# Kernel tuning notes

Measured on AMD Instinct MI355X. Metric: run time of the kernel, lower is better.

Reference implementation:

```python
import jax, jax.numpy as jnp
import numpy as np

H = 16      # heads
D = 64      # head_dim
C = 64      # k_centroid
HID = H * D
TAU1 = 1.0
TAU2 = 1.0


def setup_inputs() -> dict:
    key = jax.random.key(0)
    ks = jax.random.split(key, 12)
    B, S = 4, 1024
    inv = 1.0 / np.sqrt(D)
    return {
        "query": jax.random.normal(ks[0], (B, S, HID), dtype=jnp.float32),
        "key": jax.random.normal(ks[1], (B, S, HID), dtype=jnp.float32),
        "value": jax.random.normal(ks[2], (B, S, HID), dtype=jnp.float32),
        "Wq": jax.random.uniform(ks[3], (D, D), jnp.float32, -inv, inv),
        "bq": jax.random.uniform(ks[4], (D,), jnp.float32, -inv, inv),
        "Wk": jax.random.uniform(ks[5], (D, D), jnp.float32, -inv, inv),
        "bk": jax.random.uniform(ks[6], (D,), jnp.float32, -inv, inv),
        "Wv": jax.random.uniform(ks[7], (D, D), jnp.float32, -inv, inv),
        "bv": jax.random.uniform(ks[8], (D,), jnp.float32, -inv, inv),
        "centroid": jax.random.uniform(ks[9], (D, C), jnp.float32, -0.5, 0.5),
        "Wfc": jax.random.uniform(ks[10], (HID, HID), jnp.float32, -1.0 / np.sqrt(HID), 1.0 / np.sqrt(HID)),
        "bfc": jax.random.uniform(ks[11], (HID,), jnp.float32, -1.0 / np.sqrt(HID), 1.0 / np.sqrt(HID)),
    }


def _forward(query, key, value, Wq, bq, Wk, bk, Wv, bv, centroid, Wfc, bfc):
    B, S, _ = query.shape
    q = query.reshape(B, S, H, D)
    k = key.reshape(B, S, H, D)
    v = value.reshape(B, S, H, D)
    # per-head linear projections (applied on last dim, nn.Linear equivalent)
    Q = jnp.einsum('nshd,de->nshe', q, Wq) + bq
    K = jnp.einsum('nshd,de->nshe', k, Wk) + bk
    V = jnp.einsum('nshd,de->nshe', v, Wv) + bv
    # VQ-style key quantization: project keys onto centroids, gumbel-softmax over codebook
    K_ = jnp.einsum('nshd,dc->nshc', K, centroid)            # [B,S,H,C]
    g1 = jax.random.gumbel(jax.random.key(42), K_.shape, dtype=K_.dtype)
    prob = jax.nn.softmax((K_ + g1) / TAU1, axis=-1)
    sto_K = jnp.einsum('nshc,dc->nshd', prob, centroid)      # prob @ centroid.T
    # gumbel-softmax attention over QK^T
    scores = jnp.einsum('nqhd,nkhd->nhqk', Q, sto_K)         # [B,H,S,S]
    g2 = jax.random.gumbel(jax.random.key(43), scores.shape, dtype=scores.dtype)
    attn = jax.nn.softmax((scores + g2) / TAU2, axis=3)
    out = jnp.einsum('nhql,nlhd->nqhd', attn, V).reshape(B, S, HID)
    return jnp.einsum('nsd,de->nse', out, Wfc) + bfc


def reference(query, key, value, Wq, bq, Wk, bk, Wv, bv, centroid, Wfc, bfc):
    return _forward(query, key, value, Wq, bq, Wk, bk, Wv, bv, centroid, Wfc, bfc)
```

## Files before the change

kernel.cpp:

```cpp
#include <hip/hip_runtime.h>
#include <hip/hip_bf16.h>
#include <cstdint>

typedef unsigned short u16;
typedef __attribute__((ext_vector_type(8))) short short8;
typedef __attribute__((ext_vector_type(4))) float f32x4;

#define LT 72
#define LOG2E 1.4426950408889634f

__device__ __forceinline__ u16 f2bf(float x) {
  __hip_bfloat16 h = __float2bfloat16(x);
  union { __hip_bfloat16 h; u16 u; } cv; cv.h = h; return cv.u;
}
__device__ __forceinline__ u16 f2bf_fast(float x) {
  uint32_t b = __float_as_uint(x);
  return (u16)((b + 0x7fffu + ((b >> 16) & 1u)) >> 16);
}
__device__ __forceinline__ float bf2f(u16 u) {
  union { u16 u; __hip_bfloat16 h; } cv; cv.u = u; return __bfloat162float(cv.h);
}
__device__ __forceinline__ float ld(const void* base, size_t i, int isb) {
  return isb ? bf2f(((const u16*)base)[i]) : ((const float*)base)[i];
}
__device__ __forceinline__ void st_out(void* base, size_t i, float v, int isb) {
  if (isb) ((u16*)base)[i] = f2bf_fast(v);
  else     ((float*)base)[i] = v;
}
__device__ __forceinline__ int probe_is_bf16(const void* q) {
  const u16* u = (const u16*)q;
  int sane = 0;
  for (int i = 0; i < 64; i++) {
    u16 x = u[2 * i];
    int e = (x >> 7) & 0xff;
    sane += (int)(((e >= 117) && (e <= 133)) || ((x & 0x7fff) == 0));
  }
  return sane >= 32;
}

__device__ __forceinline__ uint32_t rotl32(uint32_t x, int n) {
  return __builtin_amdgcn_alignbit(x, x, (uint32_t)(32 - n));
}
__device__ __forceinline__ void threefry4x(uint32_t k1, uint32_t x1base,
                                           uint32_t out[4]) {
  const uint32_t ks2 = k1 ^ 0x1BD11BDAu;
  uint32_t x0[4], x1[4];
  #pragma unroll
  for (int j = 0; j < 4; j++) { x0[j] = 0u; x1[j] = x1base + ((uint32_t)j << 4); }
#define R4(rot) \
  _Pragma("unroll") \
  for (int j = 0; j < 4; j++) { \
    x0[j] += x1[j]; x1[j] = rotl32(x1[j], rot); x1[j] ^= x0[j]; \
  }
  R4(13) R4(15) R4(26) R4(6)
  #pragma unroll
  for (int j = 0; j < 4; j++) { x0[j] += k1; x1[j] += ks2 + 1u; }
  R4(17) R4(29) R4(16) R4(24)
  #pragma unroll
  for (int j = 0; j < 4; j++) { x0[j] += ks2; x1[j] += 2u; }
  R4(13) R4(15) R4(26) R4(6)
  #pragma unroll
  for (int j = 0; j < 4; j++) { x1[j] += k1 + 3u; }
  R4(17) R4(29) R4(16) R4(24)
  #pragma unroll
  for (int j = 0; j < 4; j++) { x0[j] += k1; x1[j] += ks2 + 4u; }
  R4(13) R4(15) R4(26) R4(6)
  #pragma unroll
  for (int j = 0; j < 4; j++) { out[j] = (x0[j] + ks2) ^ (x1[j] + 5u); }
#undef R4
}
__device__ __forceinline__ float rcp_l2n(uint32_t bits) {
  float u = __uint_as_float(0x3f800000u | (bits >> 9)) - 1.0f;
  float l2n = -__log2f(u);
  float t = 1.0f - u;
  float fix = fmaf(0.5f * t, t, t) * LOG2E;
  l2n = (bits >= 0xFF000000u) ? fix : l2n;
  return __builtin_amdgcn_rcpf(l2n);
}
__device__ __forceinline__ float qsum(float v) {
  v += __shfl_xor(v, 1, 64);
  v += __shfl_xor(v, 2, 64);
  v += __shfl_xor(v, 4, 64);
  v += __shfl_xor(v, 8, 64);
  return v;
}
__device__ __forceinline__ void stage_tile(u16* dst, const u16* src,
                                           int src_stride, int tid) {
  #pragma unroll
  for (int i = 0; i < 2; i++) {
    int u = tid + (i << 8);
    int r = u >> 3, c8 = (u & 7) * 8;
    *(short8*)&dst[r * LT + c8] =
        *(const short8*)&src[(size_t)r * src_stride + c8];
  }
}
__device__ __forceinline__ void pf_tile(short8 regs[2], const u16* src,
                                        int src_stride, int tid) {
  #pragma unroll
  for (int i = 0; i < 2; i++) {
    int u = tid + (i << 8);
    int r = u >> 3, c8 = (u & 7) * 8;
    regs[i] = *(const short8*)&src[(size_t)r * src_stride + c8];
  }
}
__device__ __forceinline__ void flush_tile(u16* dst, const short8 regs[2],
                                           int tid) {
  #pragma unroll
  for (int i = 0; i < 2; i++) {
    int u = tid + (i << 8);
    int r = u >> 3, c8 = (u & 7) * 8;
    *(short8*)&dst[r * LT + c8] = regs[i];
  }
}
__device__ __forceinline__ void stage_x(u16* dst, const void* src, size_t base,
                                        int isb, int tid) {
  if (isb) {
    const u16* s = (const u16*)src;
    #pragma unroll
    for (int i = 0; i < 2; i++) {
      int u = tid + (i << 8);
      int r = u >> 3, c8 = (u & 7) * 8;
      *(short8*)&dst[r * LT + c8] =
          *(const short8*)&s[base + (size_t)r * 1024 + c8];
    }
  } else {
    const float* s = (const float*)src;
    #pragma unroll
    for (int i = 0; i < 4; i++) {
      int f = (tid + (i << 8)) << 2;
      int r = f >> 6, c = f & 63;
      float4 v = *(const float4*)&s[base + (size_t)r * 1024 + c];
      ushort4 w4 = {f2bf_fast(v.x), f2bf_fast(v.y), f2bf_fast(v.z),
                    f2bf_fast(v.w)};
      *(ushort4*)&dst[r * LT + c] = w4;
    }
  }
}
__device__ __forceinline__ void gemm16(const u16* A, const u16* Bt, int w,
                                       int qd, int n, f32x4 acc[4]) {
  short8 a0 = *(const short8*)&A[(16 * w + n) * LT + qd * 8];
  short8 a1 = *(const short8*)&A[(16 * w + n) * LT + qd * 8 + 32];
  #pragma unroll
  for (int ct = 0; ct < 4; ct++) {
    short8 b0 = *(const short8*)&Bt[(16 * ct + n) * LT + qd * 8];
    short8 b1 = *(const short8*)&Bt[(16 * ct + n) * LT + qd * 8 + 32];
    acc[ct] = __builtin_amdgcn_mfma_f32_16x16x32_bf16(a0, b0, acc[ct], 0, 0, 0);
    acc[ct] = __builtin_amdgcn_mfma_f32_16x16x32_bf16(a1, b1, acc[ct], 0, 0, 0);
  }
}

__global__ __launch_bounds__(256, 4) void prep_kernel(
    const void* query, const void* Wq, const void* Wk, const void* Wv,
    const void* cen, const void* Wfc,
    const void* bq, const void* bk, const void* bv, const void* bfc,
    u16* WqT, u16* WkT, u16* WvT, u16* cenT, u16* cenN, u16* WfcT,
    float* biasF, int* flagp) {
  __shared__ __align__(16) u16 T[64 * LT];
  __shared__ int sflag;
  int tid = threadIdx.x, bid = blockIdx.x;
  if (tid == 0) sflag = probe_is_bf16(query);
  __syncthreads();
  int isb = sflag;

  if (bid < 256) {
    int k0 = (bid >> 4) * 64, c0 = (bid & 15) * 64;
    if (isb) {
      const u16* s = (const u16*)Wfc;
      #pragma unroll
      for (int i = 0; i < 2; i++) {
        int u = tid + (i << 8);
        int r = u >> 3, c8 = (u & 7) * 8;
        short8 v = *(const short8*)&s[(size_t)(k0 + r) * 1024 + c0 + c8];
        #pragma unroll
        for (int e = 0; e < 8; e++) T[(c8 + e) * LT + r] = (u16)v[e];
      }
    } else {
      const float* s = (const float*)Wfc;
      #pragma unroll
      for (int i = 0; i < 4; i++) {
        int f = (tid + (i << 8)) << 2;
        int r = f >> 6, c = f & 63;
        float4 v = *(const float4*)&s[(size_t)(k0 + r) * 1024 + c0 + c];
        T[(c + 0) * LT + r] = f2bf(v.x);
        T[(c + 1) * LT + r] = f2bf(v.y);
        T[(c + 2) * LT + r] = f2bf(v.z);
        T[(c + 3) * LT + r] = f2bf(v.w);
      }
    }
    __syncthreads();
    #pragma unroll
    for (int i = 0; i < 2; i++) {
      int u = tid + (i << 8);
      int cr = u >> 3, k8 = (u & 7) * 8;
      *(short8*)&WfcT[(size_t)(c0 + cr) * 1024 + k0 + k8] =
          *(const short8*)&T[cr * LT + k8];
    }
  } else if (bid < 259) {
    const void* W = (bid == 256) ? Wq : ((bid == 257) ? Wk : Wv);
    u16* WT = (bid == 256) ? WqT : ((bid == 257) ? WkT : WvT);
    float scl = (bid == 256) ? LOG2E : 1.0f;
    #pragma unroll
    for (int i = 0; i < 16; i++) {
      int f = tid + (i << 8);
      int r = f >> 6, c = f & 63;
      T[c * LT + r] = f2bf(ld(W, f, isb) * scl);
    }
    __syncthreads();
    #pragma unroll
    for (int i = 0; i < 16; i++) {
      int f = tid + (i << 8);
      WT[f] = T[(f >> 6) * LT + (f & 63)];
    }
  } else if (bid == 259) {
    #pragma unroll
    for (int i = 0; i < 16; i++) {
      int f = tid + (i << 8);
      int d = f >> 6, c = f & 63;
      float v = ld(cen, f, isb);
      cenN[f] = f2bf(v);
      T[c * LT + d] = f2bf(v * LOG2E);
    }
    __syncthreads();
    #pragma unroll
    for (int i = 0; i < 16; i++) {
      int f = tid + (i << 8);
      cenT[f] = T[(f >> 6) * LT + (f & 63)];
    }
  } else {
    if (tid < 64) {
      biasF[tid] = ld(bq, tid, isb) * LOG2E;
      biasF[64 + tid] = ld(bk, tid, isb);
      biasF[128 + tid] = ld(bv, tid, isb);
    }
    #pragma unroll
    for (int j = 0; j < 4; j++) {
      int c = tid + (j << 8);
      biasF[192 + c] = ld(bfc, c, isb);
    }
    if (tid == 0) *flagp = isb;
  }
}

__global__ __launch_bounds__(256, 4) void proj_kernel(
    const void* q_in, const void* k_in, const void* v_in,
    const u16* WqT, const u16* WkT, const u16* WvT,
    const u16* cenT, const u16* cenN, const float* biasF, const int* flagp,
    u16* Qbf, u16* Kbf, u16* VTbf) {
  __shared__ __align__(16) u16 XB[64 * LT], WB[64 * LT], CT[64 * LT], CN[64 * LT];
  int tid = threadIdx.x;
  int w = tid >> 6, ln = tid & 63, qd = ln >> 4, n = ln & 15;
  int bh = blockIdx.x >> 4, st = blockIdx.x & 15;
  int b = bh >> 4, h = bh & 15, s0 = st * 64;
  int isb = *flagp;
  size_t xbase = ((size_t)(b * 1024 + s0)) * 1024 + h * 64;
  size_t obase = (size_t)bh * 65536 + (size_t)s0 * 64;
  f32x4 z = {0.f, 0.f, 0.f, 0.f};

  stage_tile(CT, cenT, 64, tid);
  stage_tile(CN, cenN, 64, tid);
  stage_tile(WB, WqT, 64, tid);
  stage_x(XB, q_in, xbase, isb, tid);
  __syncthreads();

  {
    f32x4 acc[4] = {z, z, z, z};
    gemm16(XB, WB, w, qd, n, acc);
    #pragma unroll
    for (int ct = 0; ct < 4; ct++) {
      int col = 16 * ct + n;
      float bia = biasF[col];
      #pragma unroll
      for (int i = 0; i < 4; i++) {
        int srow = 16 * w + 4 * qd + i;
        Qbf[obase + (size_t)srow * 64 + col] = f2bf_fast(acc[ct][i] + bia);
      }
    }
  }
  __syncthreads();
  stage_tile(WB, WkT, 64, tid);
  stage_x(XB, k_in, xbase, isb, tid);
  __syncthreads();

  {
    f32x4 acc[4] = {z, z, z, z};
    gemm16(XB, WB, w, qd, n, acc);
    #pragma unroll
    for (int ct = 0; ct < 4; ct++) {
      int col = 16 * ct + n;
      float bia = biasF[64 + col];
      #pragma unroll
      for (int i = 0; i < 4; i++)
        XB[(16 * w + 4 * qd + i) * LT + col] = f2bf_fast(acc[ct][i] + bia);
    }
    f32x4 kc[4] = {z, z, z, z};
    gemm16(XB, CT, w, qd, n, kc);
    __syncthreads();
    uint32_t idxb42 = (((((uint32_t)b << 10) |
                         (uint32_t)(s0 + 16 * w + 4 * qd)) << 10) |
                       ((uint32_t)h << 6) | (uint32_t)n) + 42u;
    float lsum[4];
    #pragma unroll
    for (int i = 0; i < 4; i++) {
      uint32_t r[4];
      threefry4x(42u, idxb42 + ((uint32_t)i << 10), r);
      float ps = 0.f;
      #pragma unroll
      for (int ct = 0; ct < 4; ct++) {
        float pv = __builtin_amdgcn_exp2f(kc[ct][i]) * rcp_l2n(r[ct]);
        ps += pv;
        WB[(16 * w + 4 * qd + i) * LT + 16 * ct + n] = f2bf_fast(pv);
      }
      lsum[i] = qsum(ps);
    }
    f32x4 sk[4] = {z, z, z, z};
    gemm16(WB, CN, w, qd, n, sk);
    #pragma unroll
    for (int i = 0; i < 4; i++) {
      float inv = __builtin_amdgcn_rcpf(lsum[i]);
      int srow = 16 * w + 4 * qd + i;
      #pragma unroll
      for (int ct = 0; ct < 4; ct++)
        Kbf[obase + (size_t)srow * 64 + 16 * ct + n] =
            f2bf_fast(sk[ct][i] * inv);
    }
  }
  __syncthreads();
  stage_tile(WB, WvT, 64, tid);
  stage_x(XB, v_in, xbase, isb, tid);
  __syncthreads();

  {
    f32x4 acc[4] = {z, z, z, z};
    gemm16(XB, WB, w, qd, n, acc);
    #pragma unroll
    for (int ct = 0; ct < 4; ct++) {
      int col = 16 * ct + n;
      float bia = biasF[128 + col];
      #pragma unroll
      for (int i = 0; i < 4; i++)
        CT[col * LT + 16 * w + 4 * qd + i] = f2bf_fast(acc[ct][i] + bia);
    }
    __syncthreads();
    #pragma unroll
    for (int i = 0; i < 2; i++) {
      int u = tid + (i << 8);
      int dr = u >> 3, c8 = (u & 7) * 8;
      *(short8*)&VTbf[(size_t)bh * 65536 + (size_t)dr * 1024 + s0 + c8] =
          *(const short8*)&CT[dr * LT + c8];
    }
  }
}

__global__ __launch_bounds__(256, 4) void attn_kernel(
    const u16* __restrict__ Qbf, const u16* __restrict__ Kbf,
    const u16* __restrict__ VTbf, u16* __restrict__ AObf) {
  __shared__ __align__(16) u16 QS[64 * LT], KS[64 * LT], VS[64 * LT], PS[64 * LT];
  int tid = threadIdx.x;
  int w = tid >> 6, ln = tid & 63, qd = ln >> 4, n = ln & 15;
  int bid = blockIdx.x;
  int xcd = bid & 7, m = bid >> 3;
  int bh = xcd + 8 * (m >> 4), qt = m & 15;
  int b = bh >> 4, h = bh & 15, q0 = qt * 64;
  f32x4 z = {0.f, 0.f, 0.f, 0.f};
  const u16* Kb = Kbf + (size_t)bh * 65536;
  const u16* Vb = VTbf + (size_t)bh * 65536;

  stage_tile(QS, Qbf + (size_t)bh * 65536 + (size_t)q0 * 64, 64, tid);

  f32x4 o[4] = {z, z, z, z};
  float lsum[4] = {0.f, 0.f, 0.f, 0.f};
  uint32_t idxb43 = (((uint32_t)bh << 20) |
                     ((uint32_t)(q0 + 16 * w + 4 * qd) << 10) | (uint32_t)n) +
                    43u;

  short8 kreg[2], vreg[2];
  pf_tile(kreg, Kb, 64, tid);
  pf_tile(vreg, Vb, 1024, tid);

  for (int lt = 0; lt < 16; lt++) {
    float rnl[4][4];
    uint32_t base43 = idxb43 + ((uint32_t)lt << 6);
    #pragma unroll
    for (int i = 0; i < 4; i++) {
      uint32_t r[4];
      threefry4x(43u, base43 + ((uint32_t)i << 10), r);
      #pragma unroll
      for (int ct = 0; ct < 4; ct++) rnl[i][ct] = rcp_l2n(r[ct]);
    }

    __syncthreads();
    flush_tile(KS, kreg, tid);
    flush_tile(VS, vreg, tid);
    if (lt < 15) {
      pf_tile(kreg, Kb + (size_t)(lt + 1) * 4096, 64, tid);
      pf_tile(vreg, Vb + (lt + 1) * 64, 1024, tid);
    }
    __syncthreads();

    f32x4 sc[4] = {z, z, z, z};
    gemm16(QS, KS, w, qd, n, sc);

    #pragma unroll
    for (int i = 0; i < 4; i++) {
      #pragma unroll
      for (int ct = 0; ct < 4; ct++) {
        float p = __builtin_amdgcn_exp2f(sc[ct][i]) * rnl[i][ct];
        lsum[i] += p;
        PS[(16 * w + 4 * qd + i) * LT + 16 * ct + n] = f2bf_fast(p);
      }
    }
    gemm16(PS, VS, w, qd, n, o);
  }

  #pragma unroll
  for (int i = 0; i < 4; i++) {
    float inv = __builtin_amdgcn_rcpf(qsum(lsum[i]));
    int qrow = q0 + 16 * w + 4 * qd + i;
    size_t rb = ((size_t)(b * 1024 + qrow)) * 1024 + h * 64;
    #pragma unroll
    for (int ct = 0; ct < 4; ct++)
      AObf[rb + 16 * ct + n] = f2bf_fast(o[ct][i] * inv);
  }
}

__global__ __launch_bounds__(256, 4) void fc_kernel(
    const u16* __restrict__ AObf, const u16* __restrict__ WfcT,
    const float* __restrict__ biasF, const int* flagp, void* __restrict__ out) {
  __shared__ __align__(16) u16 AS[64 * LT], WS[64 * LT];
  int tid = threadIdx.x;
  int w = tid >> 6, ln = tid & 63, qd = ln >> 4, n = ln & 15;
  int r0 = (blockIdx.x >> 4) * 64, c0 = (blockIdx.x & 15) * 64;
  int isb = *flagp;
  f32x4 z = {0.f, 0.f, 0.f, 0.f};
  f32x4 acc[4] = {z, z, z, z};
  const u16* Ab = AObf + (size_t)r0 * 1024;
  const u16* Wb = WfcT + (size_t)c0 * 1024;

  short8 areg[2], wreg[2];
  pf_tile(areg, Ab, 1024, tid);
  pf_tile(wreg, Wb, 1024, tid);

  for (int kt = 0; kt < 16; kt++) {
    __syncthreads();
    flush_tile(AS, areg, tid);
    flush_tile(WS, wreg, tid);
    if (kt < 15) {
      pf_tile(areg, Ab + (kt + 1) * 64, 1024, tid);
      pf_tile(wreg, Wb + (kt + 1) * 64, 1024, tid);
    }
    __syncthreads();
    gemm16(AS, WS, w, qd, n, acc);
  }
  const float* bfcF = biasF + 192;
  #pragma unroll
  for (int ct = 0; ct < 4; ct++) {
    int col = c0 + 16 * ct + n;
    float bia = bfcF[col];
    #pragma unroll
    for (int i = 0; i < 4; i++) {
      int row = r0 + 16 * w + 4 * qd + i;
      st_out(out, (size_t)row * 1024 + col, acc[ct][i] + bia, isb);
    }
  }
}

extern "C" void kernel_launch(void* const* d_in, const int* in_sizes, int n_in,
                              void* d_out, int out_size, void* d_ws,
                              size_t ws_size, hipStream_t stream) {
  (void)in_sizes; (void)n_in; (void)out_size; (void)ws_size;
  const void* query = d_in[0];
  const void* key   = d_in[1];
  const void* value = d_in[2];
  const void* Wq = d_in[3]; const void* bq = d_in[4];
  const void* Wk = d_in[5]; const void* bk = d_in[6];
  const void* Wv = d_in[7]; const void* bv = d_in[8];
  const void* cen = d_in[9];
  const void* Wfc = d_in[10]; const void* bfc = d_in[11];

  u16* ws = (u16*)d_ws;
  u16* Qbf  = ws;
  u16* Kbf  = Qbf + 4194304;
  u16* VTbf = Kbf + 4194304;
  u16* AObf = VTbf + 4194304;
  u16* WfcT = AObf + 4194304;
  u16* WqTp = WfcT + 1048576;
  u16* WkTp = WqTp + 4096;
  u16* WvTp = WkTp + 4096;
  u16* cenTp = WvTp + 4096;
  u16* cenNp = cenTp + 4096;
  float* biasF = (float*)(cenNp + 4096);
  int* flagp = (int*)(biasF + 1216);

  prep_kernel<<<261, 256, 0, stream>>>(query, Wq, Wk, Wv, cen, Wfc, bq, bk, bv,
                                       bfc, WqTp, WkTp, WvTp, cenTp, cenNp,
                                       WfcT, biasF, flagp);
  proj_kernel<<<1024, 256, 0, stream>>>(query, key, value, WqTp, WkTp, WvTp,
                                        cenTp, cenNp, biasF, flagp,
                                        Qbf, Kbf, VTbf);
  attn_kernel<<<1024, 256, 0, stream>>>(Qbf, Kbf, VTbf, AObf);
  fc_kernel<<<1024, 256, 0, stream>>>(AObf, WfcT, biasF, flagp, d_out);
}
```

Before: 301.6 us.

## Precompute Gumbel noise in a separate kernel and stream it into attention

Moves the threefry-based Gumbel noise generation for the attention scores out of the attention loop into a dedicated kernel. That kernel writes the exponentiated noise factors to a large workspace buffer. A new attention kernel prefetches these factors per key tile alongside K/V and multiplies them into exp2 of the scores. The goal is to take the RNG arithmetic off the MFMA-bound inner loop, at the cost of writing and reading back about 256 MB of noise per call. The new path is used only when the workspace is large enough.

```diff
diff --git a/kernel.cpp b/kernel.cpp
--- a/kernel.cpp
+++ b/kernel.cpp
@@ -351,6 +351,110 @@
   }
 }
 
+__global__ __launch_bounds__(256, 8) void gumbel_kernel(
+    float* __restrict__ rnlws) {
+  int tid = threadIdx.x;
+  int w = tid >> 6, ln = tid & 63, qd = ln >> 4, n = ln & 15;
+  int bid2 = blockIdx.x;
+  int orig = bid2 >> 2, lt0 = (bid2 & 3) << 2;
+  int xcd = orig & 7, m = orig >> 3;
+  int bh = xcd + 8 * (m >> 4), qt = m & 15;
+  int q0 = qt * 64;
+  uint32_t idxb43 = (((uint32_t)bh << 20) |
+                     ((uint32_t)(q0 + 16 * w + 4 * qd) << 10) | (uint32_t)n) +
+                    43u;
+  float* base = rnlws + (((size_t)orig * 16 + lt0) * 256 + tid) * 16;
+  #pragma unroll
+  for (int t = 0; t < 4; t++) {
+    uint32_t base43 = idxb43 + ((uint32_t)(lt0 + t) << 6);
+    #pragma unroll
+    for (int i = 0; i < 4; i++) {
+      uint32_t r[4];
+      threefry4x(43u, base43 + ((uint32_t)i << 10), r);
+      float4 v;
+      v.x = rcp_l2n(r[0]); v.y = rcp_l2n(r[1]);
+      v.z = rcp_l2n(r[2]); v.w = rcp_l2n(r[3]);
+      *(float4*)(base + (size_t)t * 4096 + i * 4) = v;
+    }
+  }
+}
+
+__global__ __launch_bounds__(256, 4) void attn_pre_kernel(
+    const u16* __restrict__ Qbf, const u16* __restrict__ Kbf,
+    const u16* __restrict__ VTbf, const float* __restrict__ rnlws,
+    u16* __restrict__ AObf) {
+  __shared__ __align__(16) u16 QS[64 * LT], KS[64 * LT], VS[64 * LT], PS[64 * LT];
+  int tid = threadIdx.x;
+  int w = tid >> 6, ln = tid & 63, qd = ln >> 4, n = ln & 15;
+  int bid = blockIdx.x;
+  int xcd = bid & 7, m = bid >> 3;
+  int bh = xcd + 8 * (m >> 4), qt = m & 15;
+  int b = bh >> 4, h = bh & 15, q0 = qt * 64;
+  f32x4 z = {0.f, 0.f, 0.f, 0.f};
+  const u16* Kb = Kbf + (size_t)bh * 65536;
+  const u16* Vb = VTbf + (size_t)bh * 65536;
+
+  stage_tile(QS, Qbf + (size_t)bh * 65536 + (size_t)q0 * 64, 64, tid);
+
+  f32x4 o[4] = {z, z, z, z};
+  float lsum[4] = {0.f, 0.f, 0.f, 0.f};
+
+  const float* rnlb = rnlws + ((size_t)bid * 16 * 256 + tid) * 16;
+  float4 rc[4], rn[4];
+  #pragma unroll
+  for (int i = 0; i < 4; i++) rc[i] = *(const float4*)(rnlb + i * 4);
+
+  short8 kreg[2], vreg[2];
+  pf_tile(kreg, Kb, 64, tid);
+  pf_tile(vreg, Vb, 1024, tid);
+
+  for (int lt = 0; lt < 16; lt++) {
+    __syncthreads();
+    flush_tile(KS, kreg, tid);
+    flush_tile(VS, vreg, tid);
+    if (lt < 15) {
+      pf_tile(kreg, Kb + (size_t)(lt + 1) * 4096, 64, tid);
+      pf_tile(vreg, Vb + (lt + 1) * 64, 1024, tid);
+      const float* rp = rnlb + (size_t)(lt + 1) * 4096;
+      #pragma unroll
+      for (int i = 0; i < 4; i++) rn[i] = *(const float4*)(rp + i * 4);
+    }
+    __syncthreads();
+
+    f32x4 sc[4] = {z, z, z, z};
+    gemm16(QS, KS, w, qd, n, sc);
+
+    #pragma unroll
+    for (int i = 0; i < 4; i++) {
+      float r0 = (i == 0) ? rc[0].x : ((i == 1) ? rc[1].x : ((i == 2) ? rc[2].x : rc[3].x));
+      float r1 = (i == 0) ? rc[0].y : ((i == 1) ? rc[1].y : ((i == 2) ? rc[2].y : rc[3].y));
+      float r2 = (i == 0) ? rc[0].z : ((i == 1) ? rc[1].z : ((i == 2) ? rc[2].z : rc[3].z));
+      float r3 = (i == 0) ? rc[0].w : ((i == 1) ? rc[1].w : ((i == 2) ? rc[2].w : rc[3].w));
+      float rr[4] = {r0, r1, r2, r3};
+      #pragma unroll
+      for (int ct = 0; ct < 4; ct++) {
+        float p = __builtin_amdgcn_exp2f(sc[ct][i]) * rr[ct];
+        lsum[i] += p;
+        PS[(16 * w + 4 * qd + i) * LT + 16 * ct + n] = f2bf_fast(p);
+      }
+    }
+    gemm16(PS, VS, w, qd, n, o);
+
+    #pragma unroll
+    for (int i = 0; i < 4; i++) rc[i] = rn[i];
+  }
+
+  #pragma unroll
+  for (int i = 0; i < 4; i++) {
+    float inv = __builtin_amdgcn_rcpf(qsum(lsum[i]));
+    int qrow = q0 + 16 * w + 4 * qd + i;
+    size_t rb = ((size_t)(b * 1024 + qrow)) * 1024 + h * 64;
+    #pragma unroll
+    for (int ct = 0; ct < 4; ct++)
+      AObf[rb + 16 * ct + n] = f2bf_fast(o[ct][i] * inv);
+  }
+}
+
 __global__ __launch_bounds__(256, 4) void attn_kernel(
     const u16* __restrict__ Qbf, const u16* __restrict__ Kbf,
     const u16* __restrict__ VTbf, u16* __restrict__ AObf) {
@@ -467,7 +571,7 @@
 extern "C" void kernel_launch(void* const* d_in, const int* in_sizes, int n_in,
                               void* d_out, int out_size, void* d_ws,
                               size_t ws_size, hipStream_t stream) {
-  (void)in_sizes; (void)n_in; (void)out_size; (void)ws_size;
+  (void)in_sizes; (void)n_in; (void)out_size;
   const void* query = d_in[0];
   const void* key   = d_in[1];
   const void* value = d_in[2];
@@ -491,12 +595,22 @@
   float* biasF = (float*)(cenNp + 4096);
   int* flagp = (int*)(biasF + 1216);
 
+  const size_t RNL_OFF = 35697664ull;
+  const size_t RNL_BYTES = 268435456ull;
+  int use_pre = (ws_size >= RNL_OFF + RNL_BYTES);
+  float* rnlws = (float*)((char*)d_ws + RNL_OFF);
+
   prep_kernel<<<261, 256, 0, stream>>>(query, Wq, Wk, Wv, cen, Wfc, bq, bk, bv,
                                        bfc, WqTp, WkTp, WvTp, cenTp, cenNp,
                                        WfcT, biasF, flagp);
   proj_kernel<<<1024, 256, 0, stream>>>(query, key, value, WqTp, WkTp, WvTp,
                                         cenTp, cenNp, biasF, flagp,
                                         Qbf, Kbf, VTbf);
-  attn_kernel<<<1024, 256, 0, stream>>>(Qbf, Kbf, VTbf, AObf);
+  if (use_pre) {
+    gumbel_kernel<<<4096, 256, 0, stream>>>(rnlws);
+    attn_pre_kernel<<<1024, 256, 0, stream>>>(Qbf, Kbf, VTbf, rnlws, AObf);
+  } else {
+    attn_kernel<<<1024, 256, 0, stream>>>(Qbf, Kbf, VTbf, AObf);
+  }
   fc_kernel<<<1024, 256, 0, stream>>>(AObf, WfcT, biasF, flagp, d_out);
 }
```

Result: no change. 304.3 us (+0.9%).
